# Optimization experiments

Measured on AMD Instinct MI355X. Metric: run time of the kernel, lower is better.

## Reference

```python
import jax, jax.numpy as jnp
import numpy as np

B_, K_, D_, L_, N_, R_ = 2, 4, 128, 4096, 16, 8


def setup_inputs() -> dict:
    key = jax.random.key(0)
    ks = jax.random.split(key, 7)
    return {
        "q_x": jax.random.normal(ks[0], (B_, K_, D_, L_), jnp.float32),
        "kv_x": jax.random.normal(ks[1], (B_, K_, D_, L_), jnp.float32),
        "x_proj_weight": jax.random.normal(ks[2], (K_, R_ + 2 * N_, D_), jnp.float32) * 0.02,
        "dt_projs_weight": jax.random.normal(ks[3], (K_, D_, R_), jnp.float32) * 0.02,
        "dt_projs_bias": jax.random.normal(ks[4], (K_, D_), jnp.float32) * 0.1,
        "A_logs": jax.random.uniform(ks[5], (K_ * D_, N_), jnp.float32),
        "Ds": jax.random.normal(ks[6], (K_ * D_,), jnp.float32),
    }


def _selective_scan(u, delta, A, Bmat, Cmat, Ds):
    # u, delta: [B,K,D,L]; A: [K,D,N]; Bmat, Cmat: [B,K,N,L]; Ds: [K,D]
    uT = jnp.moveaxis(u, -1, 0)      # [L,B,K,D]
    dT = jnp.moveaxis(delta, -1, 0)  # [L,B,K,D]
    BT = jnp.moveaxis(Bmat, -1, 0)   # [L,B,K,N]
    CT = jnpp if False else jnp.moveaxis(Cmat, -1, 0)  # [L,B,K,N]
    h0 = jnp.zeros(u.shape[:3] + (A.shape[-1],), jnp.float32)  # [B,K,D,N]

    def step(h, xs):
        u_l, d_l, B_l, C_l = xs
        dA = jnp.exp(d_l[..., None] * A)  # [B,K,D,N]
        h = dA * h + (d_l * u_l)[..., None] * B_l[:, :, None, :]
        y = jnp.einsum('bkdn,bkn->bkd', h, C_l)
        return h, y

    _, yT = jax.lax.scan(step, h0, (uT, dT, BT, CT))
    y = jnp.moveaxis(yT, 0, -1)  # [B,K,D,L]
    return y + u * Ds[None, :, :, None]


def reference(q_x, kv_x, x_proj_weight, dt_projs_weight, dt_projs_bias, A_logs, Ds):
    B, K, D, L = kv_x.shape
    N = A_logs.shape[1]
    R = dt_projs_weight.shape[2]
    # projections of kv (for dt, B) and q (for C)
    x_dbl = jnp.einsum('bkdl,kcd->bkcl', kv_x, x_proj_weight)
    x_c = jnp.einsum('bkdl,kcd->bkcl', q_x, x_proj_weight)
    dts = x_dbl[:, :, :R]          # [B,K,R,L]
    Bs = x_dbl[:, :, R:R + N]      # [B,K,N,L]
    Cs = x_c[:, :, R + N:]         # [B,K,N,L]
    dts = jnp.einsum('bkrl,kdr->bkdl', dts, dt_projs_weight)
    A = -jnp.exp(A_logs.astype(jnp.float32)).reshape(K, D, N)
    delta = jax.nn.softplus(dts.astype(jnp.float32) + dt_projs_bias.astype(jnp.float32)[None, :, :, None])
    y = _selective_scan(kv_x.astype(jnp.float32), delta, A,
                        Bs.astype(jnp.float32), Cs.astype(jnp.float32),
                        Ds.astype(jnp.float32).reshape(K, D))
    return y  # [B,K,D,L] float32
```

## Files before the change

kernel.cpp:

```cpp
#include <hip/hip_runtime.h>
#include <cmath>

namespace {
constexpr int B_ = 2, K_ = 4, D_ = 128, L_ = 4096, N_ = 16, R_ = 8, C_ = 40;
constexpr int CHUNK = 32, NCH = L_ / CHUNK;
constexpr float LOG2E = 1.44269504f;
}

#if __has_builtin(__builtin_amdgcn_exp2f)
#define FEXP2(x) __builtin_amdgcn_exp2f(x)
#else
#define FEXP2(x) exp2f(x)
#endif

__global__ __launch_bounds__(640, 2) void k1_proj(
    const float* __restrict__ qx, const float* __restrict__ kv,
    const float* __restrict__ xw,
    float* __restrict__ dtsT,
    float* __restrict__ BT,
    float* __restrict__ CT)
{
    __shared__ float Wt[D_ * C_];

    const int tid = threadIdx.x;
    const int w = tid >> 6, lane = tid & 63;
    const int dg = lane >> 5, lq = lane & 31;
    int blk = blockIdx.x;
    const int lt = blk & 31; blk >>= 5;
    const int k = blk & 3; const int b = blk >> 2;
    const int bk = b * K_ + k;

    for (int i = tid; i < C_ * D_; i += 640) {
        const int c = i >> 7, d = i & 127;
        Wt[d * C_ + c] = xw[(k * C_ + c) * D_ + d];
    }
    __syncthreads();

    const float* xsrc = (w >= 6) ? qx : kv;
    const int c0 = w * 4;
    float acc[4][4];
    #pragma unroll
    for (int c = 0; c < 4; ++c)
        #pragma unroll
        for (int j = 0; j < 4; ++j) acc[c][j] = 0.f;

    const float* src = xsrc + ((size_t)bk * D_ + dg * 64) * L_ + lt * 128 + 4 * lq;
    #pragma unroll 8
    for (int dd = 0; dd < 64; ++dd) {
        const float4 x = *(const float4*)(src + (size_t)dd * L_);
        const float4 wv = *(const float4*)&Wt[(dg * 64 + dd) * C_ + c0];
        const float* wp = (const float*)&wv;
        #pragma unroll
        for (int c = 0; c < 4; ++c) {
            acc[c][0] = fmaf(x.x, wp[c], acc[c][0]);
            acc[c][1] = fmaf(x.y, wp[c], acc[c][1]);
            acc[c][2] = fmaf(x.z, wp[c], acc[c][2]);
            acc[c][3] = fmaf(x.w, wp[c], acc[c][3]);
        }
    }

    #pragma unroll
    for (int c = 0; c < 4; ++c)
        #pragma unroll
        for (int j = 0; j < 4; ++j)
            acc[c][j] += __shfl_xor(acc[c][j], 32, 64);

    if (dg == 0) {
        #pragma unroll
        for (int j = 0; j < 4; ++j) {
            const int l = lt * 128 + 4 * lq + j;
            float4 o; o.x = acc[0][j]; o.y = acc[1][j]; o.z = acc[2][j]; o.w = acc[3][j];
            if (w < 2)
                *(float4*)(dtsT + ((size_t)bk * L_ + l) * R_ + w * 4) = o;
            else if (w < 6)
                *(float4*)(BT + ((size_t)bk * L_ + l) * N_ + (w - 2) * 4) = o;
            else
                *(float4*)(CT + ((size_t)bk * L_ + l) * N_ + (w - 6) * 4) = o;
        }
    }
}

__global__ __launch_bounds__(128, 1) void k2_pass1(
    const float* __restrict__ kv, const float* __restrict__ dtsT,
    const float* __restrict__ BT, const float* __restrict__ alg,
    const float* __restrict__ dtw, const float* __restrict__ dtb,
    float* __restrict__ hend, float* __restrict__ Ssum)
{
    __shared__ float dts_s[CHUNK * R_];
    __shared__ float B_s[CHUNK * N_];

    const int tid = threadIdx.x;
    const int d = tid;
    const int blk = blockIdx.x;
    const int ch = blk & (NCH - 1);
    const int bk = blk >> 7;
    const int k = bk & 3;

    {
        const float* src = dtsT + ((size_t)bk * L_ + ch * CHUNK) * R_;
        if (tid < 64) *(float4*)&dts_s[4 * tid] = *(const float4*)(src + 4 * tid);
        const float* bsrc = BT + ((size_t)bk * L_ + ch * CHUNK) * N_;
        *(float4*)&B_s[4 * tid] = *(const float4*)(bsrc + 4 * tid);
    }

    float uu[CHUNK];
    {
        const float4* up = (const float4*)(kv + ((size_t)bk * D_ + d) * L_ + ch * CHUNK);
        #pragma unroll
        for (int j = 0; j < 8; ++j) {
            const float4 v = up[j];
            uu[4*j] = v.x; uu[4*j+1] = v.y; uu[4*j+2] = v.z; uu[4*j+3] = v.w;
        }
    }

    float dtwr[R_];
    {
        const float* p = dtw + ((size_t)k * D_ + d) * R_;
        *(float4*)&dtwr[0] = *(const float4*)p;
        *(float4*)&dtwr[4] = *(const float4*)(p + 4);
    }
    const float bias = dtb[k * D_ + d];
    float A2[N_];
    {
        const float* ap = alg + ((size_t)k * D_ + d) * N_;
        #pragma unroll
        for (int j = 0; j < 4; ++j) {
            float4 a = *(const float4*)(ap + 4 * j);
            A2[4*j]   = -__expf(a.x) * LOG2E; A2[4*j+1] = -__expf(a.y) * LOG2E;
            A2[4*j+2] = -__expf(a.z) * LOG2E; A2[4*j+3] = -__expf(a.w) * LOG2E;
        }
    }
    __syncthreads();

    float h[N_];
    #pragma unroll
    for (int n = 0; n < N_; ++n) h[n] = 0.f;
    float sd = 0.f;

    #pragma unroll
    for (int l = 0; l < CHUNK; ++l) {
        float dv[R_];
        *(float4*)&dv[0] = *(const float4*)&dts_s[l * R_];
        *(float4*)&dv[4] = *(const float4*)&dts_s[l * R_ + 4];
        float s = bias;
        #pragma unroll
        for (int r = 0; r < R_; ++r) s = fmaf(dv[r], dtwr[r], s);
        const float e = FEXP2(s * LOG2E);
        const float dlt = (s > 15.f) ? s : __logf(1.f + e);
        sd += dlt;
        const float xb = dlt * uu[l];
        #pragma unroll
        for (int g = 0; g < 4; ++g) {
            const float4 bg = *(const float4*)&B_s[l * N_ + 4 * g];
            h[4*g+0] = fmaf(FEXP2(dlt * A2[4*g+0]), h[4*g+0], xb * bg.x);
            h[4*g+1] = fmaf(FEXP2(dlt * A2[4*g+1]), h[4*g+1], xb * bg.y);
            h[4*g+2] = fmaf(FEXP2(dlt * A2[4*g+2]), h[4*g+2], xb * bg.z);
            h[4*g+3] = fmaf(FEXP2(dlt * A2[4*g+3]), h[4*g+3], xb * bg.w);
        }
    }

    float* hp = hend + (((size_t)bk * NCH + ch) * D_ + d) * N_;
    #pragma unroll
    for (int j = 0; j < 4; ++j) {
        float4 o; o.x = h[4*j]; o.y = h[4*j+1]; o.z = h[4*j+2]; o.w = h[4*j+3];
        *(float4*)(hp + 4 * j) = o;
    }
    Ssum[((size_t)bk * NCH + ch) * D_ + d] = sd;
}

__global__ __launch_bounds__(64, 2) void k25_chain(
    const float* __restrict__ alg, const float* __restrict__ Ssum,
    const float* __restrict__ hend, float* __restrict__ hinit)
{
    const int tg = blockIdx.x * 64 + threadIdx.x;
    const int n = tg & 15;
    const int d = (tg >> 4) & 127;
    const int bk = tg >> 11;
    const int k = bk & 3;

    const float A2 = -__expf(alg[((size_t)k * D_ + d) * N_ + n]) * LOG2E;
    float h = 0.f;
    for (int c0 = 0; c0 < NCH; c0 += 32) {
        float he[32], ss[32];
        #pragma unroll
        for (int j = 0; j < 32; ++j) {
            const size_t si = ((size_t)bk * NCH + c0 + j) * D_ + d;
            he[j] = hend[si * N_ + n];
            ss[j] = Ssum[si];
        }
        #pragma unroll
        for (int j = 0; j < 32; ++j) {
            const size_t si = ((size_t)bk * NCH + c0 + j) * D_ + d;
            hinit[si * N_ + n] = h;
            h = fmaf(FEXP2(ss[j] * A2), h, he[j]);
        }
    }
}

__global__ __launch_bounds__(128, 1) void k3_pass2(
    const float* __restrict__ kv, const float* __restrict__ dtsT,
    const float* __restrict__ BT, const float* __restrict__ CT,
    const float* __restrict__ alg, const float* __restrict__ dtw,
    const float* __restrict__ dtb, const float* __restrict__ DsG,
    const float* __restrict__ hinit, float* __restrict__ out)
{
    constexpr int YS = CHUNK + 1;
    __shared__ float dts_s[CHUNK * R_];
    __shared__ float B_s[CHUNK * N_];
    __shared__ float C_s[CHUNK * N_];
    __shared__ float y_s[D_ * YS];

    const int tid = threadIdx.x;
    const int d = tid;
    const int blk = blockIdx.x;
    const int ch = blk & (NCH - 1);
    const int bk = blk >> 7;
    const int k = bk & 3;

    {
        const float* src = dtsT + ((size_t)bk * L_ + ch * CHUNK) * R_;
        if (tid < 64) *(float4*)&dts_s[4 * tid] = *(const float4*)(src + 4 * tid);
        const float* bsrc = BT + ((size_t)bk * L_ + ch * CHUNK) * N_;
        *(float4*)&B_s[4 * tid] = *(const float4*)(bsrc + 4 * tid);
        const float* csrc = CT + ((size_t)bk * L_ + ch * CHUNK) * N_;
        *(float4*)&C_s[4 * tid] = *(const float4*)(csrc + 4 * tid);
    }

    float uu[CHUNK];
    {
        const float4* up = (const float4*)(kv + ((size_t)bk * D_ + d) * L_ + ch * CHUNK);
        #pragma unroll
        for (int j = 0; j < 8; ++j) {
            const float4 v = up[j];
            uu[4*j] = v.x; uu[4*j+1] = v.y; uu[4*j+2] = v.z; uu[4*j+3] = v.w;
        }
    }

    float dtwr[R_];
    {
        const float* p = dtw + ((size_t)k * D_ + d) * R_;
        *(float4*)&dtwr[0] = *(const float4*)p;
        *(float4*)&dtwr[4] = *(const float4*)(p + 4);
    }
    const float bias = dtb[k * D_ + d];
    const float Dv = DsG[k * D_ + d];
    float A2[N_];
    {
        const float* ap = alg + ((size_t)k * D_ + d) * N_;
        #pragma unroll
        for (int j = 0; j < 4; ++j) {
            float4 a = *(const float4*)(ap + 4 * j);
            A2[4*j]   = -__expf(a.x) * LOG2E; A2[4*j+1] = -__expf(a.y) * LOG2E;
            A2[4*j+2] = -__expf(a.z) * LOG2E; A2[4*j+3] = -__expf(a.w) * LOG2E;
        }
    }

    float h[N_];
    {
        const float* hp = hinit + (((size_t)bk * NCH + ch) * D_ + d) * N_;
        #pragma unroll
        for (int j = 0; j < 4; ++j) {
            float4 v = *(const float4*)(hp + 4 * j);
            h[4*j] = v.x; h[4*j+1] = v.y; h[4*j+2] = v.z; h[4*j+3] = v.w;
        }
    }
    __syncthreads();

    #pragma unroll
    for (int l = 0; l < CHUNK; ++l) {
        float dv[R_];
        *(float4*)&dv[0] = *(const float4*)&dts_s[l * R_];
        *(float4*)&dv[4] = *(const float4*)&dts_s[l * R_ + 4];
        float s = bias;
        #pragma unroll
        for (int r = 0; r < R_; ++r) s = fmaf(dv[r], dtwr[r], s);
        const float e = FEXP2(s * LOG2E);
        const float dlt = (s > 15.f) ? s : __logf(1.f + e);
        const float xb = dlt * uu[l];
        float p0 = 0.f, p1 = 0.f;
        #pragma unroll
        for (int g = 0; g < 4; ++g) {
            const float4 bg = *(const float4*)&B_s[l * N_ + 4 * g];
            const float4 cg = *(const float4*)&C_s[l * N_ + 4 * g];
            h[4*g+0] = fmaf(FEXP2(dlt * A2[4*g+0]), h[4*g+0], xb * bg.x);
            p0 = fmaf(h[4*g+0], cg.x, p0);
            h[4*g+1] = fmaf(FEXP2(dlt * A2[4*g+1]), h[4*g+1], xb * bg.y);
            p1 = fmaf(h[4*g+1], cg.y, p1);
            h[4*g+2] = fmaf(FEXP2(dlt * A2[4*g+2]), h[4*g+2], xb * bg.z);
            p0 = fmaf(h[4*g+2], cg.z, p0);
            h[4*g+3] = fmaf(FEXP2(dlt * A2[4*g+3]), h[4*g+3], xb * bg.w);
            p1 = fmaf(h[4*g+3], cg.w, p1);
        }
        y_s[d * YS + l] = fmaf(uu[l], Dv, p0 + p1);
    }
    __syncthreads();

    #pragma unroll
    for (int p = 0; p < 8; ++p) {
        const int f = tid + p * 128;
        const int row = f >> 3, j4 = (f & 7) * 4;
        const float* yp = &y_s[row * YS + j4];
        float4 o; o.x = yp[0]; o.y = yp[1]; o.z = yp[2]; o.w = yp[3];
        *(float4*)(out + ((size_t)bk * D_ + row) * L_ + ch * CHUNK + j4) = o;
    }
}

extern "C" void kernel_launch(void* const* d_in, const int* in_sizes, int n_in,
                              void* d_out, int out_size, void* d_ws, size_t ws_size,
                              hipStream_t stream)
{
    const float* qx  = (const float*)d_in[0];
    const float* kv  = (const float*)d_in[1];
    const float* xw  = (const float*)d_in[2];
    const float* dtw = (const float*)d_in[3];
    const float* dtb = (const float*)d_in[4];
    const float* alg = (const float*)d_in[5];
    const float* Ds  = (const float*)d_in[6];
    float* out = (float*)d_out;

    const size_t sz_dts = (size_t)B_ * K_ * L_ * R_;
    const size_t sz_bc  = (size_t)B_ * K_ * L_ * N_;
    const size_t sz_h   = (size_t)B_ * K_ * NCH * D_ * N_;
    const size_t sz_ss  = (size_t)B_ * K_ * NCH * D_;
    const size_t need = (sz_dts + 2 * sz_bc + 2 * sz_h + sz_ss) * sizeof(float);
    if (ws_size < need) return;

    float* dts   = (float*)d_ws;
    float* BTp   = dts + sz_dts;
    float* CTp   = BTp + sz_bc;
    float* hend  = CTp + sz_bc;
    float* hinit = hend + sz_h;
    float* Ssm   = hinit + sz_h;

    k1_proj<<<B_ * K_ * 32, 640, 0, stream>>>(qx, kv, xw, dts, BTp, CTp);
    k2_pass1<<<B_ * K_ * NCH, 128, 0, stream>>>(kv, dts, BTp, alg, dtw, dtb, hend, Ssm);
    k25_chain<<<256, 64, 0, stream>>>(alg, Ssm, hend, hinit);
    k3_pass2<<<B_ * K_ * NCH, 128, 0, stream>>>(kv, dts, BTp, CTp, alg, dtw, dtb, Ds, hinit, out);
}
```

Measured before the change: 63.74 us.

## Split inter-chunk state chain into two-level hierarchical scan

Replaces the single serial chain over all 128 chunks with a two-level scan. Groups of 16 chunks are scanned locally in parallel, a short chain runs over the 8 group ends, and pass2 combines the local prefix with the group carry-in using the decay exp(Sloc*A). This shortens the serial dependency of the chain kernel and gives it more parallelism. The cost is an extra kernel launch, more workspace traffic, and extra exp/fma work plus loads in pass2.

```diff
diff --git a/kernel.cpp b/kernel.cpp
--- a/kernel.cpp
+++ b/kernel.cpp
@@ -4,6 +4,7 @@
 namespace {
 constexpr int B_ = 2, K_ = 4, D_ = 128, L_ = 4096, N_ = 16, R_ = 8, C_ = 40;
 constexpr int CHUNK = 32, NCH = L_ / CHUNK;
+constexpr int SGC = 16, NSG = NCH / SGC;
 constexpr float LOG2E = 1.44269504f;
 }
 
@@ -16,9 +17,7 @@
 __global__ __launch_bounds__(640, 2) void k1_proj(
     const float* __restrict__ qx, const float* __restrict__ kv,
     const float* __restrict__ xw,
-    float* __restrict__ dtsT,
-    float* __restrict__ BT,
-    float* __restrict__ CT)
+    float* __restrict__ dtsT, float* __restrict__ BT, float* __restrict__ CT)
 {
     __shared__ float Wt[D_ * C_];
 
@@ -168,9 +167,45 @@
     Ssum[((size_t)bk * NCH + ch) * D_ + d] = sd;
 }
 
-__global__ __launch_bounds__(64, 2) void k25_chain(
+__global__ __launch_bounds__(64, 4) void k25a_local(
     const float* __restrict__ alg, const float* __restrict__ Ssum,
-    const float* __restrict__ hend, float* __restrict__ hinit)
+    const float* __restrict__ hend,
+    float* __restrict__ hloc, float* __restrict__ Sloc,
+    float* __restrict__ hsg_end, float* __restrict__ Ssg)
+{
+    const int tg = blockIdx.x * 64 + threadIdx.x;
+    const int n  = tg & 15;
+    const int d  = (tg >> 4) & 127;
+    const int sg = (tg >> 11) & (NSG - 1);
+    const int bk = tg >> 14;
+    const int k  = bk & 3;
+
+    const float A2 = -__expf(alg[((size_t)k * D_ + d) * N_ + n]) * LOG2E;
+
+    float he[SGC], ss[SGC];
+    #pragma unroll
+    for (int j = 0; j < SGC; ++j) {
+        const size_t si = ((size_t)bk * NCH + sg * SGC + j) * D_ + d;
+        he[j] = hend[si * N_ + n];
+        ss[j] = Ssum[si];
+    }
+    float h = 0.f, s = 0.f;
+    #pragma unroll
+    for (int j = 0; j < SGC; ++j) {
+        const size_t si = ((size_t)bk * NCH + sg * SGC + j) * D_ + d;
+        hloc[si * N_ + n] = h;
+        if (n == 0) Sloc[si] = s;
+        h = fmaf(FEXP2(ss[j] * A2), h, he[j]);
+        s += ss[j];
+    }
+    const size_t gi = ((size_t)bk * NSG + sg) * D_ + d;
+    hsg_end[gi * N_ + n] = h;
+    if (n == 0) Ssg[gi] = s;
+}
+
+__global__ __launch_bounds__(64, 4) void k25b_chain(
+    const float* __restrict__ alg, const float* __restrict__ Ssg,
+    const float* __restrict__ hsg_end, float* __restrict__ hsg_init)
 {
     const int tg = blockIdx.x * 64 + threadIdx.x;
     const int n = tg & 15;
@@ -179,21 +214,19 @@
     const int k = bk & 3;
 
     const float A2 = -__expf(alg[((size_t)k * D_ + d) * N_ + n]) * LOG2E;
+    float he[NSG], ss[NSG];
+    #pragma unroll
+    for (int j = 0; j < NSG; ++j) {
+        const size_t gi = ((size_t)bk * NSG + j) * D_ + d;
+        he[j] = hsg_end[gi * N_ + n];
+        ss[j] = Ssg[gi];
+    }
     float h = 0.f;
-    for (int c0 = 0; c0 < NCH; c0 += 32) {
-        float he[32], ss[32];
-        #pragma unroll
-        for (int j = 0; j < 32; ++j) {
-            const size_t si = ((size_t)bk * NCH + c0 + j) * D_ + d;
-            he[j] = hend[si * N_ + n];
-            ss[j] = Ssum[si];
-        }
-        #pragma unroll
-        for (int j = 0; j < 32; ++j) {
-            const size_t si = ((size_t)bk * NCH + c0 + j) * D_ + d;
-            hinit[si * N_ + n] = h;
-            h = fmaf(FEXP2(ss[j] * A2), h, he[j]);
-        }
+    #pragma unroll
+    for (int j = 0; j < NSG; ++j) {
+        const size_t gi = ((size_t)bk * NSG + j) * D_ + d;
+        hsg_init[gi * N_ + n] = h;
+        h = fmaf(FEXP2(ss[j] * A2), h, he[j]);
     }
 }
 
@@ -202,14 +235,14 @@
     const float* __restrict__ BT, const float* __restrict__ CT,
     const float* __restrict__ alg, const float* __restrict__ dtw,
     const float* __restrict__ dtb, const float* __restrict__ DsG,
-    const float* __restrict__ hinit, float* __restrict__ out)
+    const float* __restrict__ hloc, const float* __restrict__ Sloc,
+    const float* __restrict__ hsg_init, float* __restrict__ out)
 {
     constexpr int YS = CHUNK + 1;
     __shared__ float dts_s[CHUNK * R_];
     __shared__ float B_s[CHUNK * N_];
     __shared__ float C_s[CHUNK * N_];
     __shared__ float y_s[D_ * YS];
-
     const int tid = threadIdx.x;
     const int d = tid;
     const int blk = blockIdx.x;
@@ -225,7 +258,6 @@
         const float* csrc = CT + ((size_t)bk * L_ + ch * CHUNK) * N_;
         *(float4*)&C_s[4 * tid] = *(const float4*)(csrc + 4 * tid);
     }
-
     float uu[CHUNK];
     {
         const float4* up = (const float4*)(kv + ((size_t)bk * D_ + d) * L_ + ch * CHUNK);
@@ -235,7 +267,6 @@
             uu[4*j] = v.x; uu[4*j+1] = v.y; uu[4*j+2] = v.z; uu[4*j+3] = v.w;
         }
     }
-
     float dtwr[R_];
     {
         const float* p = dtw + ((size_t)k * D_ + d) * R_;
@@ -254,14 +285,19 @@
             A2[4*j+2] = -__expf(a.z) * LOG2E; A2[4*j+3] = -__expf(a.w) * LOG2E;
         }
     }
-
     float h[N_];
     {
-        const float* hp = hinit + (((size_t)bk * NCH + ch) * D_ + d) * N_;
+        const float Sp = Sloc[((size_t)bk * NCH + ch) * D_ + d];
+        const float* hp = hloc + (((size_t)bk * NCH + ch) * D_ + d) * N_;
+        const float* hg = hsg_init + (((size_t)bk * NSG + (ch >> 4)) * D_ + d) * N_;
         #pragma unroll
         for (int j = 0; j < 4; ++j) {
-            float4 v = *(const float4*)(hp + 4 * j);
-            h[4*j] = v.x; h[4*j+1] = v.y; h[4*j+2] = v.z; h[4*j+3] = v.w;
+            float4 vp = *(const float4*)(hp + 4 * j);
+            float4 vg = *(const float4*)(hg + 4 * j);
+            h[4*j+0] = fmaf(FEXP2(Sp * A2[4*j+0]), vg.x, vp.x);
+            h[4*j+1] = fmaf(FEXP2(Sp * A2[4*j+1]), vg.y, vp.y);
+            h[4*j+2] = fmaf(FEXP2(Sp * A2[4*j+2]), vg.z, vp.z);
+            h[4*j+3] = fmaf(FEXP2(Sp * A2[4*j+3]), vg.w, vp.w);
         }
     }
     __syncthreads();
@@ -281,15 +317,15 @@
         #pragma unroll
         for (int g = 0; g < 4; ++g) {
             const float4 bg = *(const float4*)&B_s[l * N_ + 4 * g];
-            const float4 cg = *(const float4*)&C_s[l * N_ + 4 * g];
+            const float4 cg4 = *(const float4*)&C_s[l * N_ + 4 * g];
             h[4*g+0] = fmaf(FEXP2(dlt * A2[4*g+0]), h[4*g+0], xb * bg.x);
-            p0 = fmaf(h[4*g+0], cg.x, p0);
+            p0 = fmaf(h[4*g+0], cg4.x, p0);
             h[4*g+1] = fmaf(FEXP2(dlt * A2[4*g+1]), h[4*g+1], xb * bg.y);
-            p1 = fmaf(h[4*g+1], cg.y, p1);
+            p1 = fmaf(h[4*g+1], cg4.y, p1);
             h[4*g+2] = fmaf(FEXP2(dlt * A2[4*g+2]), h[4*g+2], xb * bg.z);
-            p0 = fmaf(h[4*g+2], cg.z, p0);
+            p0 = fmaf(h[4*g+2], cg4.z, p0);
             h[4*g+3] = fmaf(FEXP2(dlt * A2[4*g+3]), h[4*g+3], xb * bg.w);
-            p1 = fmaf(h[4*g+3], cg.w, p1);
+            p1 = fmaf(h[4*g+3], cg4.w, p1);
         }
         y_s[d * YS + l] = fmaf(uu[l], Dv, p0 + p1);
     }
@@ -322,18 +358,28 @@
     const size_t sz_bc  = (size_t)B_ * K_ * L_ * N_;
     const size_t sz_h   = (size_t)B_ * K_ * NCH * D_ * N_;
     const size_t sz_ss  = (size_t)B_ * K_ * NCH * D_;
-    const size_t need = (sz_dts + 2 * sz_bc + 2 * sz_h + sz_ss) * sizeof(float);
+    const size_t sz_hg  = (size_t)B_ * K_ * NSG * D_ * N_;
+    const size_t sz_sg  = (size_t)B_ * K_ * NSG * D_;
+    const size_t need = (sz_dts + 2 * sz_bc + 2 * sz_h + 2 * sz_ss
+                         + 2 * sz_hg + sz_sg) * sizeof(float);
     if (ws_size < need) return;
 
-    float* dts   = (float*)d_ws;
-    float* BTp   = dts + sz_dts;
-    float* CTp   = BTp + sz_bc;
-    float* hend  = CTp + sz_bc;
-    float* hinit = hend + sz_h;
-    float* Ssm   = hinit + sz_h;
+    float* dts     = (float*)d_ws;
+    float* BTp     = dts + sz_dts;
+    float* CTp     = BTp + sz_bc;
+    float* hend    = CTp + sz_bc;
+    float* hloc    = hend + sz_h;
+    float* Ssm     = hloc + sz_h;
+    float* SlocB   = Ssm + sz_ss;
+    float* hsgEnd  = SlocB + sz_ss;
+    float* hsgInit = hsgEnd + sz_hg;
+    float* SsgB    = hsgInit + sz_hg;
 
     k1_proj<<<B_ * K_ * 32, 640, 0, stream>>>(qx, kv, xw, dts, BTp, CTp);
     k2_pass1<<<B_ * K_ * NCH, 128, 0, stream>>>(kv, dts, BTp, alg, dtw, dtb, hend, Ssm);
-    k25_chain<<<256, 64, 0, stream>>>(alg, Ssm, hend, hinit);
-    k3_pass2<<<B_ * K_ * NCH, 128, 0, stream>>>(kv, dts, BTp, CTp, alg, dtw, dtb, Ds, hinit, out);
-}
+    k25a_local<<<B_ * K_ * NSG * D_ * N_ / 64, 64, 0, stream>>>(alg, Ssm, hend,
+                                                                hloc, SlocB, hsgEnd, SsgB);
+    k25b_chain<<<256, 64, 0, stream>>>(alg, SsgB, hsgEnd, hsgInit);
+    k3_pass2<<<B_ * K_ * NCH, 128, 0, stream>>>(kv, dts, BTp, CTp, alg, dtw, dtb,
+                                                Ds, hloc, SlocB, hsgInit, out);
+}
```

New measurement: 66.62 us. +4.5%, slower.

## Write scan outputs directly from registers and split projection stores across lanes

Applied to the files above, without the earlier changes.

In the pass-2 kernel, each thread now writes its per-row outputs straight to global memory as float4 every four timesteps. This replaces staging them in a padded shared-memory tile followed by a barrier and a cooperative write, removing the shared buffer and the extra sync. Each thread's stores now hit a different row, so the store pattern is less coalesced. The projection kernel also has both lane halves store two of the four results after the shuffle reduction instead of only one half storing all four, and its inner loop unroll factor is raised from 8 to 16.

```diff
diff --git a/kernel.cpp b/kernel.cpp
--- a/kernel.cpp
+++ b/kernel.cpp
@@ -16,9 +16,7 @@
 __global__ __launch_bounds__(640, 2) void k1_proj(
     const float* __restrict__ qx, const float* __restrict__ kv,
     const float* __restrict__ xw,
-    float* __restrict__ dtsT,
-    float* __restrict__ BT,
-    float* __restrict__ CT)
+    float* __restrict__ dtsT, float* __restrict__ BT, float* __restrict__ CT)
 {
     __shared__ float Wt[D_ * C_];
 
@@ -45,7 +43,7 @@
         for (int j = 0; j < 4; ++j) acc[c][j] = 0.f;
 
     const float* src = xsrc + ((size_t)bk * D_ + dg * 64) * L_ + lt * 128 + 4 * lq;
-    #pragma unroll 8
+    #pragma unroll 16
     for (int dd = 0; dd < 64; ++dd) {
         const float4 x = *(const float4*)(src + (size_t)dd * L_);
         const float4 wv = *(const float4*)&Wt[(dg * 64 + dd) * C_ + c0];
@@ -65,18 +63,17 @@
         for (int j = 0; j < 4; ++j)
             acc[c][j] += __shfl_xor(acc[c][j], 32, 64);
 
-    if (dg == 0) {
-        #pragma unroll
-        for (int j = 0; j < 4; ++j) {
-            const int l = lt * 128 + 4 * lq + j;
-            float4 o; o.x = acc[0][j]; o.y = acc[1][j]; o.z = acc[2][j]; o.w = acc[3][j];
-            if (w < 2)
-                *(float4*)(dtsT + ((size_t)bk * L_ + l) * R_ + w * 4) = o;
-            else if (w < 6)
-                *(float4*)(BT + ((size_t)bk * L_ + l) * N_ + (w - 2) * 4) = o;
-            else
-                *(float4*)(CT + ((size_t)bk * L_ + l) * N_ + (w - 6) * 4) = o;
-        }
+    #pragma unroll
+    for (int jj = 0; jj < 2; ++jj) {
+        const int j = dg * 2 + jj;
+        const int l = lt * 128 + 4 * lq + j;
+        float4 o; o.x = acc[0][j]; o.y = acc[1][j]; o.z = acc[2][j]; o.w = acc[3][j];
+        if (w < 2)
+            *(float4*)(dtsT + ((size_t)bk * L_ + l) * R_ + w * 4) = o;
+        else if (w < 6)
+            *(float4*)(BT + ((size_t)bk * L_ + l) * N_ + (w - 2) * 4) = o;
+        else
+            *(float4*)(CT + ((size_t)bk * L_ + l) * N_ + (w - 6) * 4) = o;
     }
 }
 
@@ -204,12 +201,9 @@
     const float* __restrict__ dtb, const float* __restrict__ DsG,
     const float* __restrict__ hinit, float* __restrict__ out)
 {
-    constexpr int YS = CHUNK + 1;
     __shared__ float dts_s[CHUNK * R_];
     __shared__ float B_s[CHUNK * N_];
     __shared__ float C_s[CHUNK * N_];
-    __shared__ float y_s[D_ * YS];
-
     const int tid = threadIdx.x;
     const int d = tid;
     const int blk = blockIdx.x;
@@ -225,7 +219,6 @@
         const float* csrc = CT + ((size_t)bk * L_ + ch * CHUNK) * N_;
         *(float4*)&C_s[4 * tid] = *(const float4*)(csrc + 4 * tid);
     }
-
     float uu[CHUNK];
     {
         const float4* up = (const float4*)(kv + ((size_t)bk * D_ + d) * L_ + ch * CHUNK);
@@ -235,7 +228,6 @@
             uu[4*j] = v.x; uu[4*j+1] = v.y; uu[4*j+2] = v.z; uu[4*j+3] = v.w;
         }
     }
-
     float dtwr[R_];
     {
         const float* p = dtw + ((size_t)k * D_ + d) * R_;
@@ -254,7 +246,6 @@
             A2[4*j+2] = -__expf(a.z) * LOG2E; A2[4*j+3] = -__expf(a.w) * LOG2E;
         }
     }
-
     float h[N_];
     {
         const float* hp = hinit + (((size_t)bk * NCH + ch) * D_ + d) * N_;
@@ -266,6 +257,8 @@
     }
     __syncthreads();
 
+    float* orow = out + ((size_t)bk * D_ + d) * L_ + ch * CHUNK;
+    float4 yv;
     #pragma unroll
     for (int l = 0; l < CHUNK; ++l) {
         float dv[R_];
@@ -281,27 +274,18 @@
         #pragma unroll
         for (int g = 0; g < 4; ++g) {
             const float4 bg = *(const float4*)&B_s[l * N_ + 4 * g];
-            const float4 cg = *(const float4*)&C_s[l * N_ + 4 * g];
+            const float4 cg4 = *(const float4*)&C_s[l * N_ + 4 * g];
             h[4*g+0] = fmaf(FEXP2(dlt * A2[4*g+0]), h[4*g+0], xb * bg.x);
-            p0 = fmaf(h[4*g+0], cg.x, p0);
+            p0 = fmaf(h[4*g+0], cg4.x, p0);
             h[4*g+1] = fmaf(FEXP2(dlt * A2[4*g+1]), h[4*g+1], xb * bg.y);
-            p1 = fmaf(h[4*g+1], cg.y, p1);
+            p1 = fmaf(h[4*g+1], cg4.y, p1);
             h[4*g+2] = fmaf(FEXP2(dlt * A2[4*g+2]), h[4*g+2], xb * bg.z);
-            p0 = fmaf(h[4*g+2], cg.z, p0);
+            p0 = fmaf(h[4*g+2], cg4.z, p0);
             h[4*g+3] = fmaf(FEXP2(dlt * A2[4*g+3]), h[4*g+3], xb * bg.w);
-            p1 = fmaf(h[4*g+3], cg.w, p1);
-        }
-        y_s[d * YS + l] = fmaf(uu[l], Dv, p0 + p1);
-    }
-    __syncthreads();
-
-    #pragma unroll
-    for (int p = 0; p < 8; ++p) {
-        const int f = tid + p * 128;
-        const int row = f >> 3, j4 = (f & 7) * 4;
-        const float* yp = &y_s[row * YS + j4];
-        float4 o; o.x = yp[0]; o.y = yp[1]; o.z = yp[2]; o.w = yp[3];
-        *(float4*)(out + ((size_t)bk * D_ + row) * L_ + ch * CHUNK + j4) = o;
+            p1 = fmaf(h[4*g+3], cg4.w, p1);
+        }
+        ((float*)&yv)[l & 3] = fmaf(uu[l], Dv, p0 + p1);
+        if ((l & 3) == 3) *(float4*)(orow + (l - 3)) = yv;
     }
 }
 
```

Result: slower. 69.80 us (+9.5%).
